# Performance work log

Measured on AMD Instinct MI355X. Metric: run time of the kernel, lower is better.

## Reference

```python
import jax, jax.numpy as jnp
import numpy as np
import math

H = 12  # num_heads
LOGIT_SCALE_MAX = math.log(1.0 / 0.01)  # ~4.60517


def setup_inputs() -> dict:
    key = jax.random.key(0)
    ks = jax.random.split(key, 4)
    L, N, C = 1024, 8, 768
    scale = (C // H) ** -0.5
    return {
        "x": jax.random.normal(ks[0], (L, N, C), jnp.float32),
        "in_proj_weight": jax.random.normal(ks[1], (3 * C, C), jnp.float32) * scale,
        "in_proj_bias": jnp.zeros((3 * C,), jnp.float32),
        "logit_scale": jnp.full((H, 1, 1), jnp.log(10.0), jnp.float32),
        "head_scale": jnp.ones((H, 1, 1), jnp.float32),
        "out_w": jax.random.normal(ks[2], (C, C), jnp.float32) * scale,
        "out_b": jnp.zeros((C,), jnp.float32),
    }


def _normalize(t, eps=1e-12):
    # torch F.normalize: x / max(||x||, eps)
    n = jnp.linalg.norm(t, axis=-1, keepdims=True)
    return t / jnp.maximum(n, eps)


def reference(x, in_proj_weight, in_proj_bias, logit_scale, head_scale, out_w, out_b):
    L, N, C = x.shape
    D = C // H
    qkv = x @ in_proj_weight.T + in_proj_bias  # (L, N, 3C)
    q, k, v = jnp.split(qkv, 3, axis=-1)

    def to_heads(t):  # (L, N, C) -> (N, H, L, D); matches view(L, N*H, D).transpose(0,1)
        return t.reshape(L, N, H, D).transpose(1, 2, 0, 3)

    q, k, v = to_heads(q), to_heads(k), to_heads(v)
    # scaled-cosine attention: cosine sim * clamped-exp learnable logit scale
    attn = jnp.einsum('nhld,nhmd->nhlm', _normalize(q), _normalize(k))  # (N,H,L,L)
    ls = jnp.exp(jnp.minimum(logit_scale, LOGIT_SCALE_MAX))  # (H,1,1)
    attn = attn * ls[None]
    attn = jax.nn.softmax(attn, axis=-1)
    o = jnp.einsum('nhlm,nhmd->nhld', attn, v)  # (N,H,L,D)
    o = o * head_scale[None]  # per-head scale
    o = o.transpose(2, 0, 1, 3).reshape(L, N, C)  # back to (L, N, C)
    return o @ out_w.T + out_b
```

## Files before the change

kernel.cpp:

```cpp
#include <hip/hip_runtime.h>
#include <stdint.h>
#include <math.h>

typedef unsigned short u16;
typedef _Float16 f16;
typedef __attribute__((ext_vector_type(4))) float f32x4;
typedef __attribute__((ext_vector_type(8))) f16 h8;
typedef __attribute__((ext_vector_type(4))) f16 h4;
typedef __attribute__((ext_vector_type(2))) f16 h2;
typedef __attribute__((ext_vector_type(2))) __fp16 fp16x2;
typedef __attribute__((ext_vector_type(2))) unsigned int u32x2;
typedef __attribute__((ext_vector_type(4))) unsigned int u32x4;
typedef __attribute__((ext_vector_type(4))) unsigned short u16x4;
typedef __attribute__((ext_vector_type(8))) unsigned short u16x8;

typedef const __attribute__((address_space(1))) u16 gas_u16;
typedef __attribute__((address_space(3))) u16 las_u16;

#define MFMA32(a,b,c) __builtin_amdgcn_mfma_f32_16x16x32_f16((a),(b),(c),0,0,0)
#define MFMA16(a,b,c) __builtin_amdgcn_mfma_f32_16x16x16f16((a),(b),(c),0,0,0)

__device__ __forceinline__ float h2f(u16 h){ f16 x; __builtin_memcpy(&x,&h,2); return (float)x; }
__device__ __forceinline__ u16 f2h(float f){ f16 x = (f16)f; u16 u; __builtin_memcpy(&u,&x,2); return u; }

__device__ __forceinline__ float fast_exp2(float x){
#if __has_builtin(__builtin_amdgcn_exp2f)
  return __builtin_amdgcn_exp2f(x);
#else
  return exp2f(x);
#endif
}

__device__ __forceinline__ h2 pkrtz(float a, float b){
  fp16x2 t = __builtin_amdgcn_cvt_pkrtz(a, b);
  h2 r; __builtin_memcpy(&r, &t, 4);
  return r;
}

#define NA4 1572864
#define NB4 442368
#define NC4 147456
__global__ __launch_bounds__(256) void cvt3_kernel(
    const float* __restrict__ a, u16* __restrict__ da,
    const float* __restrict__ b, u16* __restrict__ db,
    const float* __restrict__ c, u16* __restrict__ dc)
{
  int i = blockIdx.x*256 + threadIdx.x;
  const float* s; u16* d; int off;
  if (i < NA4)            { s = a; d = da; off = i; }
  else if (i < NA4+NB4)   { s = b; d = db; off = i - NA4; }
  else if (i < NA4+NB4+NC4){ s = c; d = dc; off = i - NA4 - NB4; }
  else return;
  f32x4 v = ((const f32x4*)s)[off];
  u16x4 o;
  o[0]=f2h(v[0]); o[1]=f2h(v[1]); o[2]=f2h(v[2]); o[3]=f2h(v[3]);
  ((u16x4*)d)[off] = o;
}

__global__ __launch_bounds__(256) void gemm_kernel(
    const u16* __restrict__ A, const u16* __restrict__ B, const float* __restrict__ bias,
    int mode, u16* __restrict__ qh, u16* __restrict__ kh, u16* __restrict__ vh,
    float* __restrict__ outp, const float* __restrict__ lsb)
{
  __shared__ u16 lA[2][128*64];
  __shared__ u16 lB[2][128*64];
  const int tid = threadIdx.x;
  const int lane = tid & 63;
  const int w = tid >> 6, wr = w >> 1, wc = w & 1;
  const int lo = lane & 15, hi = lane >> 4;

  const int bx = blockIdx.x, by = blockIdx.y;

  f32x4 zero = {0.f,0.f,0.f,0.f};
  f32x4 acc[4][4];
#pragma unroll
  for (int a=0;a<4;a++)
#pragma unroll
    for (int b=0;b<4;b++) acc[a][b] = zero;
  const u16* Ag = A + (size_t)bx*128*768;
  const u16* Bg = B + (size_t)by*128*768;
  const int srow = tid >> 3;
  const int scol = (((tid & 7) ^ (srow & 7)) * 8);

#define STAGE(buf, kt) do { \
    _Pragma("unroll") \
    for (int j=0;j<4;j++) { \
      __builtin_amdgcn_global_load_lds((gas_u16*)(Ag + (size_t)(j*32+srow)*768 + (kt) + scol), (las_u16*)(&lA[buf][j*2048 + tid*8]), 16, 0, 0); \
      __builtin_amdgcn_global_load_lds((gas_u16*)(Bg + (size_t)(j*32+srow)*768 + (kt) + scol), (las_u16*)(&lB[buf][j*2048 + tid*8]), 16, 0, 0); \
    } \
  } while(0)

  STAGE(0, 0);
#pragma unroll
  for (int t = 0; t < 12; ++t) {
    const int cur = t & 1;
    if (t < 11) {
      STAGE(cur^1, (t+1)*64);
      asm volatile("s_waitcnt vmcnt(8)" ::: "memory");
    } else {
      asm volatile("s_waitcnt vmcnt(0)" ::: "memory");
    }
    __builtin_amdgcn_sched_barrier(0);
    __builtin_amdgcn_s_barrier();
#pragma unroll
    for (int kk=0;kk<2;kk++) {
      h8 af[4], bfr[4];
#pragma unroll
      for (int mf=0; mf<4; mf++) {
        int r = wr*64 + mf*16 + lo;
        af[mf]  = *(const h8*)(&lA[cur][r*64 + (((hi + 4*kk) ^ (lo & 7)) * 8)]);
      }
#pragma unroll
      for (int nf=0; nf<4; nf++) {
        int r = wc*64 + nf*16 + lo;
        bfr[nf] = *(const h8*)(&lB[cur][r*64 + (((hi + 4*kk) ^ (lo & 7)) * 8)]);
      }
#pragma unroll
      for (int mf=0; mf<4; mf++)
#pragma unroll
        for (int nf=0; nf<4; nf++)
          acc[mf][nf] = MFMA32(af[mf], bfr[nf], acc[mf][nf]);
    }
    asm volatile("s_waitcnt lgkmcnt(0)" ::: "memory");
    __builtin_amdgcn_sched_barrier(0);
    __builtin_amdgcn_s_barrier();
  }
#undef STAGE

  const int r0 = bx*128 + wr*64;
  const int j0 = by*128 + wc*64;
  if (mode == 0) {
    const int p = (j0 >= 1536) ? 2 : ((j0 >= 768) ? 1 : 0);
    const int c0 = j0 - p*768;
    const int hh = c0 >> 6;
    u16* dst = (p==0) ? qh : ((p==1) ? kh : vh);
    float bi[4];
#pragma unroll
    for (int nf=0;nf<4;nf++) bi[nf] = bias[j0 + nf*16 + lo];
    float qsc = 1.0f;
    if (p == 0) qsc = __expf(fminf(lsb[hh], 4.6051701859880913680f)) * 1.4426950408889634f;
    const bool dnorm = (p != 2);
#pragma unroll
    for (int mf=0; mf<4; mf++)
#pragma unroll
      for (int i=0;i<4;i++) {
        int r = r0 + mf*16 + 4*hi + i;
        int n = r & 7, l = r >> 3;
        float v[4]; float ss = 0.f;
#pragma unroll
        for (int nf=0;nf<4;nf++){ v[nf] = acc[mf][nf][i] + bi[nf]; ss += v[nf]*v[nf]; }
        float sc = 1.0f;
        if (dnorm) {
          ss += __shfl_xor(ss, 1);
          ss += __shfl_xor(ss, 2);
          ss += __shfl_xor(ss, 4);
          ss += __shfl_xor(ss, 8);
          sc = qsc / fmaxf(sqrtf(ss), 1e-12f);
        }
        size_t base = (((size_t)n*12 + hh)*1024 + l)*64;
#pragma unroll
        for (int nf=0;nf<4;nf++)
          dst[base + nf*16 + lo] = f2h(v[nf]*sc);
      }
  } else {
#pragma unroll
    for (int nf=0; nf<4; nf++) {
      int j = j0 + nf*16 + lo;
      float bi = bias[j];
#pragma unroll
      for (int mf=0; mf<4; mf++)
#pragma unroll
        for (int i=0;i<4;i++) {
          int r = r0 + mf*16 + 4*hi + i;
          outp[(size_t)r*768 + j] = acc[mf][nf][i] + bi;
        }
    }
  }
}

__global__ __launch_bounds__(256) void transpose_kernel(const u16* __restrict__ vh, u16* __restrict__ vt){
  __shared__ u16 tile[64*72];
  const int nh = blockIdx.y, lt = blockIdx.x, tid = threadIdx.x;
  const int r = tid >> 2, c0 = (tid & 3) * 16;
  const u16* src = vh + (size_t)nh*65536 + (size_t)(lt*64 + r)*64 + c0;
  u32x4 a = *(const u32x4*)src, b = *(const u32x4*)(src + 8);
  *(u32x4*)(tile + r*72 + c0)     = a;
  *(u32x4*)(tile + r*72 + c0 + 8) = b;
  __syncthreads();
  u16x8 o0, o1;
#pragma unroll
  for (int s=0;s<8;s++){ o0[s] = tile[(c0+s)*72 + r]; o1[s] = tile[(c0+8+s)*72 + r]; }
  u16* dst = vt + (size_t)nh*65536 + (size_t)r*1024 + lt*64 + c0;
  *(u16x8*)dst       = o0;
  *(u16x8*)(dst + 8) = o1;
}

__global__ __launch_bounds__(256, 6) void flash_kernel(
    const u16* __restrict__ qh, const u16* __restrict__ kh, const u16* __restrict__ vt,
    u16* __restrict__ obuf, const float* __restrict__ hsv, const float* __restrict__ lsp)
{
  __shared__ u16 lK[64*64];
  __shared__ u16 lVT[64*64];
  const int lin = blockIdx.y*16 + blockIdx.x;
  const int xcd = lin & 7, g = lin >> 3;
  const int nh = xcd + 8*(g >> 4);
  const int qt = g & 15;
  const int h = nh % 12, n = nh / 12;
  const u16* Qp = qh + (size_t)nh*65536;
  const u16* Kp = kh + (size_t)nh*65536;
  const u16* Vp = vt + (size_t)nh*65536;
  const int tid = threadIdx.x, lane = tid & 63, w = tid >> 6;
  const int lo = lane & 15, hi = lane >> 4;
  const int e = lo & 7;

  h8 qa0, qa1;
  {
    const u16* qrow = Qp + (size_t)(qt*64 + w*16 + lo)*64 + hi*8;
    qa0 = *(const h8*)qrow;
    qa1 = *(const h8*)(qrow + 32);
  }
  const f32x4 zero = {0.f,0.f,0.f,0.f};
  f32x4 oA[4] = {zero,zero,zero,zero};
  f32x4 lA4 = zero;
  const h4 ones = {(f16)1.f,(f16)1.f,(f16)1.f,(f16)1.f};

  float OFF;
  {
    float b = __expf(fminf(lsp[h], 4.6051701859880913680f)) * 1.4426950408889634f;
    OFF = fmaxf(b - 15.5f, 0.f);
  }

  const int sr = tid >> 2;
  const int c4 = tid & 3;
  const int sx1 = sr & 7;
  const int sx2 = (sr & 7) << 1;

  u32x4 ka, kb, va, vb;
  ka = *(const u32x4*)(Kp + (size_t)sr*64 + c4*16);
  kb = *(const u32x4*)(Kp + (size_t)sr*64 + c4*16 + 8);
  va = *(const u32x4*)(Vp + (size_t)sr*1024 + c4*16);
  vb = *(const u32x4*)(Vp + (size_t)sr*1024 + c4*16 + 8);

  for (int t = 0; t < 16; ++t) {
    {
      u16* kr = lK + sr*64;
      *(u32x4*)(kr + (((2*c4)   ^ sx1) << 3)) = ka;
      *(u32x4*)(kr + (((2*c4+1) ^ sx1) << 3)) = kb;
      u16* vr = lVT + sr*64;
      *(u32x2*)(vr + (((( 0|c4) ^ sx2) << 2))) = (u32x2){va[0], va[1]};
      *(u32x2*)(vr + (((( 4|c4) ^ sx2) << 2))) = (u32x2){va[2], va[3]};
      *(u32x2*)(vr + (((( 8|c4) ^ sx2) << 2))) = (u32x2){vb[0], vb[1]};
      *(u32x2*)(vr + ((((12|c4) ^ sx2) << 2))) = (u32x2){vb[2], vb[3]};
    }
    asm volatile("s_waitcnt lgkmcnt(0)" ::: "memory");
    __builtin_amdgcn_sched_barrier(0);
    __builtin_amdgcn_s_barrier();
    if (t < 15) {
      ka = *(const u32x4*)(Kp + (size_t)(t+1)*4096 + (size_t)sr*64 + c4*16);
      kb = *(const u32x4*)(Kp + (size_t)(t+1)*4096 + (size_t)sr*64 + c4*16 + 8);
      va = *(const u32x4*)(Vp + (size_t)sr*1024 + (t+1)*64 + c4*16);
      vb = *(const u32x4*)(Vp + (size_t)sr*1024 + (t+1)*64 + c4*16 + 8);
    }
    f32x4 sa[4];
#pragma unroll
    for (int kf=0; kf<4; kf++) {
      const u16* krow = lK + (kf*16 + lo)*64;
      h8 k0 = *(const h8*)(krow + (((hi  ) ^ e) << 3));
      h8 k1 = *(const h8*)(krow + (((hi+4) ^ e) << 3));
      sa[kf] = MFMA32(k1, qa1, MFMA32(k0, qa0, zero));
    }
    if (OFF != 0.f) {
#pragma unroll
      for (int kf=0;kf<4;kf++)
#pragma unroll
        for (int i=0;i<4;i++) sa[kf][i] -= OFF;
    }
    h4 pa[4];
#pragma unroll
    for (int kf=0;kf<4;kf++) {
      h2 a01 = pkrtz(fast_exp2(sa[kf][0]), fast_exp2(sa[kf][1]));
      h2 a23 = pkrtz(fast_exp2(sa[kf][2]), fast_exp2(sa[kf][3]));
      pa[kf] = __builtin_shufflevector(a01, a23, 0, 1, 2, 3);
    }
#pragma unroll
    for (int kf=0;kf<4;kf++) lA4 = MFMA16(ones, pa[kf], lA4);
#pragma unroll
    for (int db=0; db<4; db++) {
      const u16* vrow = lVT + (db*16 + lo)*64;
      h8 v01 = *(const h8*)(vrow + ((((2*hi  ) ^ e) << 3)));
      h8 v23 = *(const h8*)(vrow + ((((2*hi+1) ^ e) << 3)));
      oA[db] = MFMA16(__builtin_shufflevector(v01, v01, 0,1,2,3), pa[0], oA[db]);
      oA[db] = MFMA16(__builtin_shufflevector(v01, v01, 4,5,6,7), pa[1], oA[db]);
      oA[db] = MFMA16(__builtin_shufflevector(v23, v23, 0,1,2,3), pa[2], oA[db]);
      oA[db] = MFMA16(__builtin_shufflevector(v23, v23, 4,5,6,7), pa[3], oA[db]);
    }
    asm volatile("s_waitcnt lgkmcnt(0)" ::: "memory");
    __builtin_amdgcn_sched_barrier(0);
    __builtin_amdgcn_s_barrier();
  }
  float inv = hsv[h] / lA4[0];
  int l = qt*64 + w*16 + lo;
  u16* dst = obuf + ((size_t)l*8 + n)*768 + h*64;
#pragma unroll
  for (int db=0; db<4; db++) {
    u16x4 pk;
#pragma unroll
    for (int i=0;i<4;i++) pk[i] = f2h(oA[db][i] * inv);
    *(u16x4*)(dst + db*16 + hi*4) = pk;
  }
}

extern "C" void kernel_launch(void* const* d_in, const int* in_sizes, int n_in,
                              void* d_out, int out_size, void* d_ws, size_t ws_size,
                              hipStream_t stream)
{
  (void)in_sizes; (void)n_in; (void)out_size; (void)ws_size;
  const float* x  = (const float*)d_in[0];
  const float* w1 = (const float*)d_in[1];
  const float* b1 = (const float*)d_in[2];
  const float* ls = (const float*)d_in[3];
  const float* hs = (const float*)d_in[4];
  const float* w2 = (const float*)d_in[5];
  const float* b2 = (const float*)d_in[6];
  float* out = (float*)d_out;

  u16* x_bf  = (u16*)d_ws;
  u16* w1_bf = x_bf  + 6291456;
  u16* w2_bf = w1_bf + 1769472;
  u16* qh    = w2_bf + 589824;
  u16* kh    = qh    + 6291456;
  u16* vh    = kh    + 6291456;
  u16* vt    = vh    + 6291456;
  u16* ob    = x_bf;

  cvt3_kernel<<<8448, 256, 0, stream>>>(x, x_bf, w1, w1_bf, w2, w2_bf);
  gemm_kernel<<<dim3(64,18), 256, 0, stream>>>(x_bf, w1_bf, b1, 0, qh, kh, vh, nullptr, ls);
  transpose_kernel<<<dim3(16,96), 256, 0, stream>>>(vh, vt);
  flash_kernel<<<dim3(16,96), 256, 0, stream>>>(qh, kh, vt, ob, hs, ls);
  gemm_kernel<<<dim3(64,6), 256, 0, stream>>>(ob, w2_bf, b2, 1, nullptr, nullptr, nullptr, out, ls);
}
```

Measured before the change: 126.0 us.

## Fuse V transpose into QKV GEMM epilogue via LDS staging

The V-projection tiles of the QKV GEMM are now staged through shared memory in a swizzled layout and written directly in transposed (d-major, L-contiguous) form. This removes the separate transpose kernel launch and the extra global write and read of the V tensor. The cost is a more complex epilogue with a block barrier and strided LDS reads in the V blocks, plus reuse of the GEMM operand buffers as scratch.

```diff
diff --git a/kernel.cpp b/kernel.cpp
--- a/kernel.cpp
+++ b/kernel.cpp
@@ -59,7 +59,7 @@
 
 __global__ __launch_bounds__(256) void gemm_kernel(
     const u16* __restrict__ A, const u16* __restrict__ B, const float* __restrict__ bias,
-    int mode, u16* __restrict__ qh, u16* __restrict__ kh, u16* __restrict__ vh,
+    int mode, u16* __restrict__ qh, u16* __restrict__ kh, u16* __restrict__ vtp,
     float* __restrict__ outp, const float* __restrict__ lsb)
 {
   __shared__ u16 lA[2][128*64];
@@ -131,37 +131,69 @@
   const int j0 = by*128 + wc*64;
   if (mode == 0) {
     const int p = (j0 >= 1536) ? 2 : ((j0 >= 768) ? 1 : 0);
-    const int c0 = j0 - p*768;
-    const int hh = c0 >> 6;
-    u16* dst = (p==0) ? qh : ((p==1) ? kh : vh);
     float bi[4];
 #pragma unroll
     for (int nf=0;nf<4;nf++) bi[nf] = bias[j0 + nf*16 + lo];
-    float qsc = 1.0f;
-    if (p == 0) qsc = __expf(fminf(lsb[hh], 4.6051701859880913680f)) * 1.4426950408889634f;
-    const bool dnorm = (p != 2);
-#pragma unroll
-    for (int mf=0; mf<4; mf++)
-#pragma unroll
-      for (int i=0;i<4;i++) {
-        int r = r0 + mf*16 + 4*hi + i;
-        int n = r & 7, l = r >> 3;
-        float v[4]; float ss = 0.f;
-#pragma unroll
-        for (int nf=0;nf<4;nf++){ v[nf] = acc[mf][nf][i] + bi[nf]; ss += v[nf]*v[nf]; }
-        float sc = 1.0f;
-        if (dnorm) {
+    if (p == 2) {
+      u16* Tt = (wc == 0) ? (u16*)lA : (u16*)lB;
+      const int cbase = wr*16;
+#pragma unroll
+      for (int mf=0; mf<4; mf++)
+#pragma unroll
+        for (int nf=0; nf<4; nf++) {
+          int d = nf*16 + lo;
+          int c = cbase + mf*4 + hi;
+          u16x4 pk;
+#pragma unroll
+          for (int i=0;i<4;i++) pk[i] = f2h(acc[mf][nf][i] + bi[nf]);
+          *(u16x4*)(Tt + d*128 + ((c ^ ((d & 7) << 2)) << 2)) = pk;
+        }
+      __syncthreads();
+      const int hh0 = 2*by - 24;
+#pragma unroll
+      for (int kq=0; kq<8; kq++) {
+        int idx = tid + kq*256;
+        int nn  = idx & 7;
+        int d   = (idx >> 3) & 63;
+        int lh  = (idx >> 9) & 1;
+        int wcc = idx >> 10;
+        const u16* Ts = (wcc == 0) ? (const u16*)lA : (const u16*)lB;
+        u16x8 v8;
+#pragma unroll
+        for (int ll=0; ll<8; ll++) {
+          int rl = (lh*8 + ll)*8 + nn;
+          int c  = rl >> 2;
+          v8[ll] = Ts[d*128 + ((c ^ ((d & 7) << 2)) << 2) + (rl & 3)];
+        }
+        size_t off = (((size_t)nn*12 + hh0 + wcc)*64 + d)*1024 + (size_t)bx*16 + lh*8;
+        *(u16x8*)(vtp + off) = v8;
+      }
+    } else {
+      const int c0 = j0 - p*768;
+      const int hh = c0 >> 6;
+      u16* dst = (p==0) ? qh : kh;
+      float qsc = 1.0f;
+      if (p == 0) qsc = __expf(fminf(lsb[hh], 4.6051701859880913680f)) * 1.4426950408889634f;
+#pragma unroll
+      for (int mf=0; mf<4; mf++)
+#pragma unroll
+        for (int i=0;i<4;i++) {
+          int r = r0 + mf*16 + 4*hi + i;
+          int n = r & 7, l = r >> 3;
+          float v[4]; float ss = 0.f;
+#pragma unroll
+          for (int nf=0;nf<4;nf++){ v[nf] = acc[mf][nf][i] + bi[nf]; ss += v[nf]*v[nf]; }
           ss += __shfl_xor(ss, 1);
           ss += __shfl_xor(ss, 2);
           ss += __shfl_xor(ss, 4);
           ss += __shfl_xor(ss, 8);
-          sc = qsc / fmaxf(sqrtf(ss), 1e-12f);
+          float sc = qsc / fmaxf(sqrtf(ss), 1e-12f);
+          size_t base = (((size_t)n*12 + hh)*1024 + l)*64;
+#pragma unroll
+          for (int nf=0;nf<4;nf++)
+            dst[base + nf*16 + lo] = f2h(v[nf]*sc);
         }
-        size_t base = (((size_t)n*12 + hh)*1024 + l)*64;
-#pragma unroll
-        for (int nf=0;nf<4;nf++)
-          dst[base + nf*16 + lo] = f2h(v[nf]*sc);
-      }
+    }
   } else {
 #pragma unroll
     for (int nf=0; nf<4; nf++) {
@@ -176,23 +208,6 @@
         }
     }
   }
-}
-
-__global__ __launch_bounds__(256) void transpose_kernel(const u16* __restrict__ vh, u16* __restrict__ vt){
-  __shared__ u16 tile[64*72];
-  const int nh = blockIdx.y, lt = blockIdx.x, tid = threadIdx.x;
-  const int r = tid >> 2, c0 = (tid & 3) * 16;
-  const u16* src = vh + (size_t)nh*65536 + (size_t)(lt*64 + r)*64 + c0;
-  u32x4 a = *(const u32x4*)src, b = *(const u32x4*)(src + 8);
-  *(u32x4*)(tile + r*72 + c0)     = a;
-  *(u32x4*)(tile + r*72 + c0 + 8) = b;
-  __syncthreads();
-  u16x8 o0, o1;
-#pragma unroll
-  for (int s=0;s<8;s++){ o0[s] = tile[(c0+s)*72 + r]; o1[s] = tile[(c0+8+s)*72 + r]; }
-  u16* dst = vt + (size_t)nh*65536 + (size_t)r*1024 + lt*64 + c0;
-  *(u16x8*)dst       = o0;
-  *(u16x8*)(dst + 8) = o1;
 }
 
 __global__ __launch_bounds__(256, 6) void flash_kernel(
@@ -329,13 +344,11 @@
   u16* w2_bf = w1_bf + 1769472;
   u16* qh    = w2_bf + 589824;
   u16* kh    = qh    + 6291456;
-  u16* vh    = kh    + 6291456;
-  u16* vt    = vh    + 6291456;
+  u16* vt    = kh    + 6291456;
   u16* ob    = x_bf;
 
   cvt3_kernel<<<8448, 256, 0, stream>>>(x, x_bf, w1, w1_bf, w2, w2_bf);
-  gemm_kernel<<<dim3(64,18), 256, 0, stream>>>(x_bf, w1_bf, b1, 0, qh, kh, vh, nullptr, ls);
-  transpose_kernel<<<dim3(16,96), 256, 0, stream>>>(vh, vt);
+  gemm_kernel<<<dim3(64,18), 256, 0, stream>>>(x_bf, w1_bf, b1, 0, qh, kh, vt, nullptr, ls);
   flash_kernel<<<dim3(16,96), 256, 0, stream>>>(qh, kh, vt, ob, hs, ls);
   gemm_kernel<<<dim3(64,6), 256, 0, stream>>>(ob, w2_bf, b2, 1, nullptr, nullptr, nullptr, out, ls);
 }
```

Result: no change. 123.7 us (-1.8%).
